# Performance work log

Hardware: AMD Instinct MI355X
Metric: run time of the kernel (lower is better)

Reference implementation:

```python
import jax, jax.numpy as jnp
import numpy as np

B, C, H, W = 64, 1, 1024, 1024
KS, F, OUT = 16, 128, 10
L = (H // KS) * (W // KS)  # 4096 non-overlapping patch locations


def setup_inputs() -> dict:
    key = jax.random.key(0)
    k1, k2, k3, k4, k5 = jax.random.split(key, 5)
    x = jax.random.normal(k1, (B, C, H, W), dtype=jnp.float32)
    weight = jax.random.normal(k2, (F, L, C, KS, KS), dtype=jnp.float32)
    bias = jax.random.normal(k3, (F, L, C), dtype=jnp.float32)
    dec_w = jax.random.normal(k4, (OUT, F * L * C), dtype=jnp.float32) * 0.01
    dec_b = jax.random.normal(k5, (OUT,), dtype=jnp.float32)
    return {"x": x, "weight": weight, "bias": bias, "dec_w": dec_w, "dec_b": dec_b}


def reference(x, weight, bias, dec_w, dec_b):
    b, c, h, w = x.shape
    f, l, cw, kh, kw = weight.shape
    # Non-overlapping unfold (stride == kernel): [B,C,H,W] -> [B, L, C, kh, kw]
    patches = x.reshape(b, c, h // kh, kh, w // kw, kw)
    patches = patches.transpose(0, 2, 4, 1, 3, 5).reshape(b, l, c, kh, kw)
    # Locally-connected multiply-sum: out[b,f,l,c] = sum_ij patches[b,l,c,i,j] * weight[f,l,c,i,j]
    y = jnp.einsum('blcij,flcij->bflc', patches, weight) + bias
    y = jax.nn.relu(y)
    y = y.reshape(b, -1)  # [B, F*L*C], f-major like torch's view
    return y @ dec_w.T + dec_b
```

## Files before the change

kernel.cpp:

```cpp
#include <hip/hip_runtime.h>
#include <hip/hip_bf16.h>

#define B_    64
#define F_    128
#define L_    4096
#define K_    256
#define OUT_  10
#define HW_   (1024 * 1024)
#define WIMG_ 1024
#define CHUNK 64
#define NCHUNK 4

typedef __attribute__((ext_vector_type(8))) short bf16x8;
typedef __attribute__((ext_vector_type(4))) float f32x4;

static __device__ __forceinline__ unsigned short f2bf(float f) {
    return __builtin_bit_cast(unsigned short, __float2bfloat16(f));
}

__global__ __launch_bounds__(256, 3)
void lcn_main(const float* __restrict__ x, const float* __restrict__ wgt,
              const float* __restrict__ bias, const float* __restrict__ dec_w,
              float* __restrict__ ws) {
    const int l  = blockIdx.x;
    const int hb = l >> 6, wb = l & 63;
    const int t  = threadIdx.x;
    const int lane = t & 63;
    const int wid  = t >> 6;
    const int wr   = wid >> 1;
    const int wc   = wid & 1;
    const int ln15 = lane & 15;
    const int kg   = lane >> 4;

    __shared__ union {
        struct { unsigned short xs[2][64 * CHUNK]; unsigned short wm[2][128 * CHUNK]; } s;
        float ysm[B_][132];
        float red[16][B_][OUT_];
    } u;

    const int sfg = t >> 4;
    const int swk = (t & 15) * 4;
    const int sxb = t >> 2;
    const int sxq = (t & 3) * 4;

    const float* xrow0 = x + (size_t)sxb * HW_ + (size_t)(hb * 16) * WIMG_ + wb * 16 + sxq;

    float4 wg[8], xg[4];

    auto LOADC = [&](int c) {
        #pragma unroll
        for (int p = 0; p < 8; ++p) {
            const int f = p * 16 + sfg;
            wg[p] = *reinterpret_cast<const float4*>(
                wgt + ((size_t)f * L_ + l) * K_ + c * CHUNK + swk);
        }
        #pragma unroll
        for (int i = 0; i < 4; ++i)
            xg[i] = *reinterpret_cast<const float4*>(xrow0 + (size_t)(c * 4 + i) * WIMG_);
    };
    auto WRITEC = [&](int buf) {
        #pragma unroll
        for (int p = 0; p < 8; ++p) {
            const int f = p * 16 + sfg;
            const int e = f * CHUNK + (swk ^ ((f & 7) << 3));
            ushort4 v = make_ushort4(f2bf(wg[p].x), f2bf(wg[p].y), f2bf(wg[p].z), f2bf(wg[p].w));
            *reinterpret_cast<ushort4*>(&u.s.wm[buf][e]) = v;
        }
        #pragma unroll
        for (int i = 0; i < 4; ++i) {
            const int k0 = i * 16 + sxq;
            const int e = sxb * CHUNK + (k0 ^ ((sxb & 7) << 3));
            ushort4 v = make_ushort4(f2bf(xg[i].x), f2bf(xg[i].y), f2bf(xg[i].z), f2bf(xg[i].w));
            *reinterpret_cast<ushort4*>(&u.s.xs[buf][e]) = v;
        }
    };

    f32x4 acc[2][4];
    #pragma unroll
    for (int m = 0; m < 2; ++m)
        #pragma unroll
        for (int n = 0; n < 4; ++n)
            acc[m][n] = (f32x4){0.f, 0.f, 0.f, 0.f};

    LOADC(0);
    WRITEC(0);
    LOADC(1);
    __syncthreads();

    int cur = 0;
    for (int c = 0; c < NCHUNK; ++c) {
        #pragma unroll
        for (int ks = 0; ks < 2; ++ks) {
            const int kbase = ks * 32 + kg * 8;
            bf16x8 a[2], bb[4];
            #pragma unroll
            for (int m = 0; m < 2; ++m) {
                const int b = wr * 32 + m * 16 + ln15;
                a[m] = *reinterpret_cast<const bf16x8*>(
                    &u.s.xs[cur][b * CHUNK + (kbase ^ ((b & 7) << 3))]);
            }
            #pragma unroll
            for (int n = 0; n < 4; ++n) {
                const int f = wc * 64 + n * 16 + ln15;
                bb[n] = *reinterpret_cast<const bf16x8*>(
                    &u.s.wm[cur][f * CHUNK + (kbase ^ ((f & 7) << 3))]);
            }
            #pragma unroll
            for (int m = 0; m < 2; ++m)
                #pragma unroll
                for (int n = 0; n < 4; ++n)
                    acc[m][n] = __builtin_amdgcn_mfma_f32_16x16x32_bf16(
                        a[m], bb[n], acc[m][n], 0, 0, 0);
        }
        if (c + 1 < NCHUNK) {
            WRITEC(cur ^ 1);
            if (c + 2 < NCHUNK) LOADC(c + 2);
        }
        __syncthreads();
        cur ^= 1;
    }

    float bv[4];
    #pragma unroll
    for (int n = 0; n < 4; ++n)
        bv[n] = bias[(size_t)(wc * 64 + n * 16 + ln15) * L_ + l];

    #pragma unroll
    for (int m = 0; m < 2; ++m)
        #pragma unroll
        for (int n = 0; n < 4; ++n)
            #pragma unroll
            for (int r = 0; r < 4; ++r) {
                const int b = wr * 32 + m * 16 + kg * 4 + r;
                const int f = wc * 64 + n * 16 + ln15;
                u.ysm[b][f] = fmaxf(acc[m][n][r] + bv[n], 0.f);
            }
    __syncthreads();

    const int tx = t & 15, ty = t >> 4;
    const int b0 = tx * 4, f0 = ty * 8;

    float yv[4][8];
    #pragma unroll
    for (int bi = 0; bi < 4; ++bi) {
        f32x4 p0 = *reinterpret_cast<const f32x4*>(&u.ysm[b0 + bi][f0]);
        f32x4 p1 = *reinterpret_cast<const f32x4*>(&u.ysm[b0 + bi][f0 + 4]);
        yv[bi][0] = p0.x; yv[bi][1] = p0.y; yv[bi][2] = p0.z; yv[bi][3] = p0.w;
        yv[bi][4] = p1.x; yv[bi][5] = p1.y; yv[bi][6] = p1.z; yv[bi][7] = p1.w;
    }
    __syncthreads();

    float part[4][OUT_];
    #pragma unroll
    for (int bi = 0; bi < 4; ++bi)
        #pragma unroll
        for (int o = 0; o < OUT_; ++o) part[bi][o] = 0.f;

    #pragma unroll
    for (int fj = 0; fj < 8; ++fj) {
        #pragma unroll
        for (int o = 0; o < OUT_; ++o) {
            const float dw = dec_w[(size_t)o * ((size_t)F_ * L_) + (size_t)(f0 + fj) * L_ + l];
            #pragma unroll
            for (int bi = 0; bi < 4; ++bi)
                part[bi][o] = fmaf(yv[bi][fj], dw, part[bi][o]);
        }
    }

    #pragma unroll
    for (int bi = 0; bi < 4; ++bi)
        #pragma unroll
        for (int o = 0; o < OUT_; ++o)
            u.red[ty][b0 + bi][o] = part[bi][o];
    __syncthreads();

    for (int idx = t; idx < B_ * OUT_; idx += 256) {
        const int b = idx / OUT_;
        const int o = idx - b * OUT_;
        float s = 0.f;
        #pragma unroll
        for (int g = 0; g < 16; ++g) s += u.red[g][b][o];
        ws[(size_t)b * ((size_t)L_ * OUT_) + (size_t)l * OUT_ + o] = s;
    }
}

__global__ __launch_bounds__(640)
void lcn_reduce(const float* __restrict__ ws, const float* __restrict__ dec_b,
                float* __restrict__ out) {
    const int b = blockIdx.x;
    const int j = threadIdx.x;
    const float* base = ws + (size_t)b * ((size_t)L_ * OUT_);

    float s = 0.f;
    #pragma unroll 8
    for (int i = 0; i < 64; ++i)
        s += base[j + i * (64 * OUT_)];

    __shared__ float lds[64 * OUT_];
    lds[j] = s;
    __syncthreads();

    if (j < OUT_) {
        float tot = dec_b[j];
        #pragma unroll
        for (int lc = 0; lc < 64; ++lc) tot += lds[lc * OUT_ + j];
        out[b * OUT_ + j] = tot;
    }
}

extern "C" void kernel_launch(void* const* d_in, const int* in_sizes, int n_in,
                              void* d_out, int out_size, void* d_ws, size_t ws_size,
                              hipStream_t stream) {
    const float* x     = (const float*)d_in[0];
    const float* wgt   = (const float*)d_in[1];
    const float* bias  = (const float*)d_in[2];
    const float* dec_w = (const float*)d_in[3];
    const float* dec_b = (const float*)d_in[4];
    float* out = (float*)d_out;
    float* wsf = (float*)d_ws;

    lcn_main<<<dim3(L_), dim3(256), 0, stream>>>(x, wgt, bias, dec_w, wsf);
    lcn_reduce<<<dim3(B_), dim3(640), 0, stream>>>(wsf, dec_b, out);
}
```

Measured before the change: 274.1 us.

## Stage full x tile in LDS and feed weights straight from global to MFMA

The whole 64x256 bf16 patch tile is loaded into LDS once up front, replacing the chunked double-buffered pipeline. Weights now go from global memory straight into registers as the MFMA B operand, skipping the LDS write and read for weights. The wave tiling changes so each wave covers all 64 batch rows and 32 filters. This removes per-chunk barriers and weight LDS traffic. In exchange, weight-load latency is no longer hidden by explicit prefetch, and each lane's global weight loads are less contiguous.

Result: faster. 267.8 us (-2.3%).

```diff
diff --git a/kernel.cpp b/kernel.cpp
--- a/kernel.cpp
+++ b/kernel.cpp
@@ -8,14 +8,20 @@
 #define OUT_  10
 #define HW_   (1024 * 1024)
 #define WIMG_ 1024
-#define CHUNK 64
-#define NCHUNK 4
 
 typedef __attribute__((ext_vector_type(8))) short bf16x8;
 typedef __attribute__((ext_vector_type(4))) float f32x4;
 
 static __device__ __forceinline__ unsigned short f2bf(float f) {
     return __builtin_bit_cast(unsigned short, __float2bfloat16(f));
+}
+static __device__ __forceinline__ bf16x8 cvt8(float4 a, float4 b) {
+    bf16x8 r;
+    r[0] = (short)f2bf(a.x); r[1] = (short)f2bf(a.y);
+    r[2] = (short)f2bf(a.z); r[3] = (short)f2bf(a.w);
+    r[4] = (short)f2bf(b.x); r[5] = (short)f2bf(b.y);
+    r[6] = (short)f2bf(b.z); r[7] = (short)f2bf(b.w);
+    return r;
 }
 
 __global__ __launch_bounds__(256, 3)
@@ -26,125 +32,94 @@
     const int hb = l >> 6, wb = l & 63;
     const int t  = threadIdx.x;
     const int lane = t & 63;
-    const int wid  = t >> 6;
-    const int wr   = wid >> 1;
-    const int wc   = wid & 1;
+    const int wc   = t >> 6;
     const int ln15 = lane & 15;
     const int kg   = lane >> 4;
 
     __shared__ union {
-        struct { unsigned short xs[2][64 * CHUNK]; unsigned short wm[2][128 * CHUNK]; } s;
+        unsigned short xs[B_ * K_];
         float ysm[B_][132];
         float red[16][B_][OUT_];
     } u;
 
-    const int sfg = t >> 4;
-    const int swk = (t & 15) * 4;
-    const int sxb = t >> 2;
-    const int sxq = (t & 3) * 4;
+    {
+        const int b  = t >> 2;
+        const int j0 = (t & 3) * 4;
+        const float* xp = x + (size_t)b * HW_ + (size_t)(hb * 16) * WIMG_ + wb * 16 + j0;
+        float4 v[16];
+        #pragma unroll
+        for (int r = 0; r < 16; ++r)
+            v[r] = *reinterpret_cast<const float4*>(xp + (size_t)r * WIMG_);
+        const int swz = (b & 7) << 3;
+        #pragma unroll
+        for (int r = 0; r < 16; ++r) {
+            const int k = r * 16 + j0;
+            ushort4 s4 = make_ushort4(f2bf(v[r].x), f2bf(v[r].y), f2bf(v[r].z), f2bf(v[r].w));
+            *reinterpret_cast<ushort4*>(&u.xs[b * K_ + (k ^ swz)]) = s4;
+        }
+    }
+    __syncthreads();
 
-    const float* xrow0 = x + (size_t)sxb * HW_ + (size_t)(hb * 16) * WIMG_ + wb * 16 + sxq;
+    const float* w0p = wgt + ((size_t)(wc * 32 + ln15) * L_ + l) * K_;
+    const float* w1p = w0p + (size_t)16 * L_ * K_;
 
-    float4 wg[8], xg[4];
+    f32x4 acc[4][2];
+    #pragma unroll
+    for (int m = 0; m < 4; ++m)
+        #pragma unroll
+        for (int n = 0; n < 2; ++n)
+            acc[m][n] = (f32x4){0.f, 0.f, 0.f, 0.f};
 
-    auto LOADC = [&](int c) {
+    #pragma unroll
+    for (int ks = 0; ks < 8; ++ks) {
+        const int kb = ks * 32 + kg * 8;
+        const float4 wa0 = *reinterpret_cast<const float4*>(w0p + kb);
+        const float4 wa1 = *reinterpret_cast<const float4*>(w0p + kb + 4);
+        const float4 wb0 = *reinterpret_cast<const float4*>(w1p + kb);
+        const float4 wb1 = *reinterpret_cast<const float4*>(w1p + kb + 4);
+        const bf16x8 b0 = cvt8(wa0, wa1);
+        const bf16x8 b1 = cvt8(wb0, wb1);
+        bf16x8 a[4];
         #pragma unroll
-        for (int p = 0; p < 8; ++p) {
-            const int f = p * 16 + sfg;
-            wg[p] = *reinterpret_cast<const float4*>(
-                wgt + ((size_t)f * L_ + l) * K_ + c * CHUNK + swk);
+        for (int m = 0; m < 4; ++m) {
+            const int b = m * 16 + ln15;
+            a[m] = *reinterpret_cast<const bf16x8*>(
+                &u.xs[b * K_ + (kb ^ ((b & 7) << 3))]);
         }
         #pragma unroll
-        for (int i = 0; i < 4; ++i)
-            xg[i] = *reinterpret_cast<const float4*>(xrow0 + (size_t)(c * 4 + i) * WIMG_);
-    };
-    auto WRITEC = [&](int buf) {
-        #pragma unroll
-        for (int p = 0; p < 8; ++p) {
-            const int f = p * 16 + sfg;
-            const int e = f * CHUNK + (swk ^ ((f & 7) << 3));
-            ushort4 v = make_ushort4(f2bf(wg[p].x), f2bf(wg[p].y), f2bf(wg[p].z), f2bf(wg[p].w));
-            *reinterpret_cast<ushort4*>(&u.s.wm[buf][e]) = v;
+        for (int m = 0; m < 4; ++m) {
+            acc[m][0] = __builtin_amdgcn_mfma_f32_16x16x32_bf16(a[m], b0, acc[m][0], 0, 0, 0);
+            acc[m][1] = __builtin_amdgcn_mfma_f32_16x16x32_bf16(a[m], b1, acc[m][1], 0, 0, 0);
         }
-        #pragma unroll
-        for (int i = 0; i < 4; ++i) {
-            const int k0 = i * 16 + sxq;
-            const int e = sxb * CHUNK + (k0 ^ ((sxb & 7) << 3));
-            ushort4 v = make_ushort4(f2bf(xg[i].x), f2bf(xg[i].y), f2bf(xg[i].z), f2bf(xg[i].w));
-            *reinterpret_cast<ushort4*>(&u.s.xs[buf][e]) = v;
-        }
-    };
+    }
 
-    f32x4 acc[2][4];
+    float bv[2];
     #pragma unroll
-    for (int m = 0; m < 2; ++m)
-        #pragma unroll
-        for (int n = 0; n < 4; ++n)
-            acc[m][n] = (f32x4){0.f, 0.f, 0.f, 0.f};
+    for (int n = 0; n < 2; ++n)
+        bv[n] = bias[(size_t)(wc * 32 + n * 16 + ln15) * L_ + l];
 
-    LOADC(0);
-    WRITEC(0);
-    LOADC(1);
     __syncthreads();
 
-    int cur = 0;
-    for (int c = 0; c < NCHUNK; ++c) {
+    #pragma unroll
+    for (int m = 0; m < 4; ++m)
         #pragma unroll
-        for (int ks = 0; ks < 2; ++ks) {
-            const int kbase = ks * 32 + kg * 8;
-            bf16x8 a[2], bb[4];
-            #pragma unroll
-            for (int m = 0; m < 2; ++m) {
-                const int b = wr * 32 + m * 16 + ln15;
-                a[m] = *reinterpret_cast<const bf16x8*>(
-                    &u.s.xs[cur][b * CHUNK + (kbase ^ ((b & 7) << 3))]);
-            }
-            #pragma unroll
-            for (int n = 0; n < 4; ++n) {
-                const int f = wc * 64 + n * 16 + ln15;
-                bb[n] = *reinterpret_cast<const bf16x8*>(
-                    &u.s.wm[cur][f * CHUNK + (kbase ^ ((f & 7) << 3))]);
-            }
-            #pragma unroll
-            for (int m = 0; m < 2; ++m)
-                #pragma unroll
-                for (int n = 0; n < 4; ++n)
-                    acc[m][n] = __builtin_amdgcn_mfma_f32_16x16x32_bf16(
-                        a[m], bb[n], acc[m][n], 0, 0, 0);
-        }
-        if (c + 1 < NCHUNK) {
-            WRITEC(cur ^ 1);
-            if (c + 2 < NCHUNK) LOADC(c + 2);
-        }
-        __syncthreads();
-        cur ^= 1;
-    }
-
-    float bv[4];
-    #pragma unroll
-    for (int n = 0; n < 4; ++n)
-        bv[n] = bias[(size_t)(wc * 64 + n * 16 + ln15) * L_ + l];
-
-    #pragma unroll
-    for (int m = 0; m < 2; ++m)
-        #pragma unroll
-        for (int n = 0; n < 4; ++n)
+        for (int n = 0; n < 2; ++n)
             #pragma unroll
             for (int r = 0; r < 4; ++r) {
-                const int b = wr * 32 + m * 16 + kg * 4 + r;
-                const int f = wc * 64 + n * 16 + ln15;
+                const int b = m * 16 + kg * 4 + r;
+                const int f = wc * 32 + n * 16 + ln15;
                 u.ysm[b][f] = fmaxf(acc[m][n][r] + bv[n], 0.f);
             }
     __syncthreads();
 
     const int tx = t & 15, ty = t >> 4;
-    const int b0 = tx * 4, f0 = ty * 8;
+    const int b0_ = tx * 4, f0_ = ty * 8;
 
     float yv[4][8];
     #pragma unroll
     for (int bi = 0; bi < 4; ++bi) {
-        f32x4 p0 = *reinterpret_cast<const f32x4*>(&u.ysm[b0 + bi][f0]);
-        f32x4 p1 = *reinterpret_cast<const f32x4*>(&u.ysm[b0 + bi][f0 + 4]);
+        f32x4 p0 = *reinterpret_cast<const f32x4*>(&u.ysm[b0_ + bi][f0_]);
+        f32x4 p1 = *reinterpret_cast<const f32x4*>(&u.ysm[b0_ + bi][f0_ + 4]);
         yv[bi][0] = p0.x; yv[bi][1] = p0.y; yv[bi][2] = p0.z; yv[bi][3] = p0.w;
         yv[bi][4] = p1.x; yv[bi][5] = p1.y; yv[bi][6] = p1.z; yv[bi][7] = p1.w;
     }
@@ -160,7 +135,7 @@
     for (int fj = 0; fj < 8; ++fj) {
         #pragma unroll
         for (int o = 0; o < OUT_; ++o) {
-            const float dw = dec_w[(size_t)o * ((size_t)F_ * L_) + (size_t)(f0 + fj) * L_ + l];
+            const float dw = dec_w[(size_t)o * ((size_t)F_ * L_) + (size_t)(f0_ + fj) * L_ + l];
             #pragma unroll
             for (int bi = 0; bi < 4; ++bi)
                 part[bi][o] = fmaf(yv[bi][fj], dw, part[bi][o]);
@@ -171,7 +146,7 @@
     for (int bi = 0; bi < 4; ++bi)
         #pragma unroll
         for (int o = 0; o < OUT_; ++o)
-            u.red[ty][b0 + bi][o] = part[bi][o];
+            u.red[ty][b0_ + bi][o] = part[bi][o];
     __syncthreads();
 
     for (int idx = t; idx < B_ * OUT_; idx += 256) {
```
